# Performance work log

Measured on AMD Instinct MI355X. Metric: run time of the kernel, lower is better.

The kernel has to match this reference:

```python
import jax, jax.numpy as jnp
import numpy as np

HEAD_DIM = 64
N_HEADS = 32
N_KV_HEADS = 8
ROPE_THETA = 10000.0
NEG_INF = -1e9


def _rope_cos_sin(position_ids, head_dim, dtype):
    # position_ids: [b, s] int -> cos/sin [b, s, head_dim]
    inv_freq = 1.0 / (ROPE_THETA ** (jnp.arange(0, head_dim, 2, dtype=jnp.float32) / head_dim))
    freqs = position_ids.astype(jnp.float32)[..., None] * inv_freq  # [b, s, d/2]
    emb = jnp.concatenate([freqs, freqs], axis=-1)                  # [b, s, d]
    return jnp.cos(emb).astype(dtype), jnp.sin(emb).astype(dtype)


def _rotate_half(x):
    half = x.shape[-1] // 2
    return jnp.concatenate([-x[..., half:], x[..., :half]], axis=-1)


def setup_inputs() -> dict:
    key = jax.random.key(0)
    ks = jax.random.split(key, 6)
    b, s, din = 2, 2048, 4096  # din = 2 * hidden_size
    hidden_states = jax.random.normal(ks[0], (b, s, din), dtype=jnp.float32)
    # additive causal mask [b, 1, q, kv]
    causal = jnp.tril(jnp.ones((s, s), dtype=bool))
    attention_mask = jnp.where(causal, 0.0, NEG_INF).astype(jnp.float32)
    attention_mask = jnp.broadcast_to(attention_mask[None, None], (b, 1, s, s))
    position_ids = jnp.broadcast_to(jnp.arange(s, dtype=jnp.int32)[None], (b, s))
    scale = 0.02
    Wq = jax.random.normal(ks[1], (din, N_HEADS * HEAD_DIM), dtype=jnp.float32) * scale
    Wk = jax.random.normal(ks[2], (din, N_KV_HEADS * HEAD_DIM), dtype=jnp.float32) * scale
    Wv = jax.random.normal(ks[3], (din, N_KV_HEADS * HEAD_DIM), dtype=jnp.float32) * scale
    Wo = jax.random.normal(ks[4], (N_HEADS * HEAD_DIM, din // 2), dtype=jnp.float32) * scale
    return {"hidden_states": hidden_states, "attention_mask": attention_mask,
            "position_ids": position_ids, "Wq": Wq, "Wk": Wk, "Wv": Wv, "Wo": Wo}


def reference(hidden_states, attention_mask, position_ids, Wq, Wk, Wv, Wo):
    b, s, _ = hidden_states.shape
    g = N_HEADS // N_KV_HEADS  # GQA group size
    q = (hidden_states @ Wq).reshape(b, s, N_HEADS, HEAD_DIM).transpose(0, 2, 1, 3)      # [b,h,s,d]
    k = (hidden_states @ Wk).reshape(b, s, N_KV_HEADS, HEAD_DIM).transpose(0, 2, 1, 3)   # [b,kh,s,d]
    v = (hidden_states @ Wv).reshape(b, s, N_KV_HEADS, HEAD_DIM).transpose(0, 2, 1, 3)
    cos, sin = _rope_cos_sin(position_ids, HEAD_DIM, q.dtype)  # [b,s,d]
    cos, sin = cos[:, None], sin[:, None]                      # [b,1,s,d]
    q = q * cos + _rotate_half(q) * sin
    k = k * cos + _rotate_half(k) * sin
    # GQA: group query heads instead of materializing repeated K/V
    qg = q.reshape(b, N_KV_HEADS, g, s, HEAD_DIM)
    scores = jnp.einsum('bhgqd,bhkd->bhgqk', qg, k) / jnp.sqrt(jnp.float32(HEAD_DIM))
    scores = scores + attention_mask[:, :, None]               # broadcast over kv-head, group
    probs = jax.nn.softmax(scores.astype(jnp.float32), axis=-1).astype(q.dtype)
    out = jnp.einsum('bhgqk,bhkd->bhgqd', probs, v)            # [b,kh,g,s,d]
    out = out.reshape(b, N_HEADS, s, HEAD_DIM).transpose(0, 2, 1, 3).reshape(b, s, N_HEADS * HEAD_DIM)
    return out @ Wo
```

## Files before the change

### kernel.cpp

```cpp
#include <hip/hip_runtime.h>
#include <hip/hip_bf16.h>
#include <cstdint>
#include <cstddef>

typedef __attribute__((ext_vector_type(4))) float floatx4;
typedef __attribute__((ext_vector_type(8))) short shortx8;

typedef __attribute__((address_space(1))) void gvoid;
typedef __attribute__((address_space(3))) void lvoid;

__device__ inline __hip_bfloat16 f2b(float x) { return __float2bfloat16(x); }
__device__ inline float b2f(__hip_bfloat16 x) { return __bfloat162float(x); }
__device__ inline unsigned short f2bu(float x) {
  __hip_bfloat16 h = __float2bfloat16(x);
  return *reinterpret_cast<unsigned short*>(&h);
}
__device__ inline unsigned cvt_pk_bf16(float lo, float hi) {
  unsigned r;
  asm("v_cvt_pk_bf16_f32 %0, %1, %2" : "=v"(r) : "v"(lo), "v"(hi));
  return r;
}

template <typename T> __device__ inline T cvt_out(float x);
template <> __device__ inline float cvt_out<float>(float x) { return x; }
template <> __device__ inline __hip_bfloat16 cvt_out<__hip_bfloat16>(float x) { return __float2bfloat16(x); }

__global__ void cvt_f32_bf16(const float* __restrict__ in, __hip_bfloat16* __restrict__ out, int n) {
  int i = (blockIdx.x * blockDim.x + threadIdx.x) * 4;
  if (i >= n) return;
  float4 v = *(const float4*)(in + i);
  __hip_bfloat16 o[4] = { f2b(v.x), f2b(v.y), f2b(v.z), f2b(v.w) };
  *(ushort4*)(out + i) = *(const ushort4*)o;
}

__global__ void transpose_cvt(const float* __restrict__ in, __hip_bfloat16* __restrict__ out, int K, int N) {
  __shared__ float tile[32][33];
  int n0 = blockIdx.x * 32, k0 = blockIdx.y * 32;
  int tx = threadIdx.x, ty = threadIdx.y;
#pragma unroll
  for (int i = 0; i < 4; i++)
    tile[ty + i * 8][tx] = in[(size_t)(k0 + ty + i * 8) * N + n0 + tx];
  __syncthreads();
#pragma unroll
  for (int i = 0; i < 4; i++)
    out[(size_t)(n0 + ty + i * 8) * K + k0 + tx] = f2b(tile[tx][ty + i * 8]);
}

template <typename OutT>
__global__ __launch_bounds__(256) void gemm_bt(
    const __hip_bfloat16* __restrict__ A,
    const __hip_bfloat16* __restrict__ Bt,
    OutT* __restrict__ C, int M, int N, int K) {
  __shared__ short lA[128 * 32];
  __shared__ short lB[128 * 32];
  const int m0 = blockIdx.x * 128, n0 = blockIdx.y * 128;
  const int t = threadIdx.x;
  const int l = t & 63;
  const int w = t >> 6;
  const int wm = (w & 1) * 64, wn = (w >> 1) * 64;
  const int lr = l & 15, lq = l >> 4;
  floatx4 acc[4][4] = {};

  for (int kt = 0; kt < K; kt += 32) {
    __syncthreads();
#pragma unroll
    for (int j = 0; j < 2; j++) {
      int flat = j * 2048 + t * 8;
      const __hip_bfloat16* srcA = A + (size_t)(m0 + (flat >> 5)) * K + kt + (flat & 31);
      __builtin_amdgcn_global_load_lds((gvoid*)srcA, (lvoid*)&lA[flat], 16, 0, 0);
      const __hip_bfloat16* srcB = Bt + (size_t)(n0 + (flat >> 5)) * K + kt + (flat & 31);
      __builtin_amdgcn_global_load_lds((gvoid*)srcB, (lvoid*)&lB[flat], 16, 0, 0);
    }
    __syncthreads();
    shortx8 af[4], bfr[4];
#pragma unroll
    for (int mi = 0; mi < 4; mi++)
      af[mi] = *(const shortx8*)&lA[(wm + mi * 16 + lr) * 32 + lq * 8];
#pragma unroll
    for (int ni = 0; ni < 4; ni++)
      bfr[ni] = *(const shortx8*)&lB[(wn + ni * 16 + lr) * 32 + lq * 8];
#pragma unroll
    for (int mi = 0; mi < 4; mi++)
#pragma unroll
      for (int ni = 0; ni < 4; ni++)
        acc[mi][ni] = __builtin_amdgcn_mfma_f32_16x16x32_bf16(af[mi], bfr[ni], acc[mi][ni], 0, 0, 0);
  }
#pragma unroll
  for (int mi = 0; mi < 4; mi++)
#pragma unroll
    for (int ni = 0; ni < 4; ni++) {
      int row = m0 + wm + mi * 16 + lq * 4;
      int col = n0 + wn + ni * 16 + lr;
#pragma unroll
      for (int r = 0; r < 4; r++)
        C[(size_t)(row + r) * N + col] = cvt_out<OutT>(acc[mi][ni][r]);
    }
}

__global__ void rope_kernel(__hip_bfloat16* __restrict__ q, int stride, float scale) {
  int i = threadIdx.x;
  int row = blockIdx.x * 8 + threadIdx.y;
  int head = blockIdx.y;
  int pos = row & 2047;
  float freq = (float)pos * exp2f(-(float)i * (13.287712379549449f / 32.0f));
  float s = sinf(freq), c = cosf(freq);
  __hip_bfloat16* p = q + (size_t)row * stride + head * 64 + i;
  float x1 = b2f(p[0]), x2 = b2f(p[32]);
  p[0]  = f2b((x1 * c - x2 * s) * scale);
  p[32] = f2b((x2 * c + x1 * s) * scale);
}

__global__ void v_transpose(const __hip_bfloat16* __restrict__ QKV, __hip_bfloat16* __restrict__ Vt) {
  __shared__ __hip_bfloat16 tile[32][33];
  int bkvh = blockIdx.z;
  int s0 = blockIdx.x * 32, d0 = blockIdx.y * 32;
  int b = bkvh >> 3, kvh = bkvh & 7;
  int tx = threadIdx.x, ty = threadIdx.y;
#pragma unroll
  for (int i = 0; i < 4; i++)
    tile[ty + i * 8][tx] = QKV[(size_t)(b * 2048 + s0 + ty + i * 8) * 3072 + 2560 + kvh * 64 + d0 + tx];
  __syncthreads();
#pragma unroll
  for (int i = 0; i < 4; i++)
    Vt[((size_t)(bkvh * 64 + d0 + ty + i * 8) << 11) + s0 + tx] = tile[tx][ty + i * 8];
}

__global__ __launch_bounds__(256, 3) void attn_kernel(
    const __hip_bfloat16* __restrict__ Qp,
    const __hip_bfloat16* __restrict__ Kp,
    const __hip_bfloat16* __restrict__ Vt,
    __hip_bfloat16* __restrict__ O) {
  __shared__ __align__(16) short lK[2][64 * 64];
  __shared__ __align__(16) short lV[2][64 * 64];
  __shared__ __align__(16) short lP[4][16 * 64];
  const int h = blockIdx.y, b = blockIdx.z;
  const int ia = ((int)blockIdx.x + (h & 15) + ((h >> 4) << 3) + (b << 2)) & 15;
  const int ib = 31 - ia;
  const int kvh = h >> 2;
  const int t = threadIdx.x, w = t >> 6, l = t & 63;
  const int lr = l & 15, lq = l >> 4;
  const int swz = lr & 7;

  const int q0A = ia * 64 + w * 16;
  const int q0B = ib * 64 + w * 16;
  const __hip_bfloat16* qpA = Qp + (size_t)(b * 2048 + q0A + lr) * 3072 + h * 64 + lq * 8;
  const __hip_bfloat16* qpB = Qp + (size_t)(b * 2048 + q0B + lr) * 3072 + h * 64 + lq * 8;
  shortx8 qfA0 = *(const shortx8*)(qpA);
  shortx8 qfA1 = *(const shortx8*)(qpA + 32);
  shortx8 qfB0 = *(const shortx8*)(qpB);
  shortx8 qfB1 = *(const shortx8*)(qpB + 32);

  const int srow = t >> 3, schunk = t & 7;
  const int swzch = schunk ^ (srow & 7);
  const __hip_bfloat16* ksrc = Kp + (size_t)(b * 2048 + srow) * 3072 + kvh * 64 + swzch * 8;
  const __hip_bfloat16* vsrc = Vt + ((size_t)((b * 8 + kvh) * 64 + srow) << 11) + swzch * 8;
  short* const myP = &lP[w][0];

  floatx4 oA[4] = {}, oB[4] = {};
  float mA = -1e30f, sumA = 0.f, mB = -1e30f, sumB = 0.f;

  const int KT = 32 - ia;

  auto stage = [&](int sbuf, int kt2) {
#pragma unroll
    for (int j = 0; j < 2; j++) {
      __builtin_amdgcn_global_load_lds((gvoid*)(ksrc + (size_t)(kt2 * 64 + j * 32) * 3072),
                                       (lvoid*)&lK[sbuf][w * 512 + j * 2048], 16, 0, 0);
      __builtin_amdgcn_global_load_lds((gvoid*)(vsrc + (size_t)(j * 32) * 2048 + kt2 * 64),
                                       (lvoid*)&lV[sbuf][w * 512 + j * 2048], 16, 0, 0);
    }
  };

  stage(0, 0);

  for (int kt = 0; kt < KT; kt++) {
    const int buf = kt & 1;
    __syncthreads();
    if (kt + 1 < KT) stage(buf ^ 1, kt + 1);
    const bool doA = (kt <= ia);

    floatx4 sA[4] = {}, sB[4] = {};
    __builtin_amdgcn_s_setprio(1);
#pragma unroll
    for (int mi = 0; mi < 4; mi++) {
      const short* kr = &lK[buf][(mi * 16 + lr) * 64];
      shortx8 kf0 = *(const shortx8*)(kr + ((lq ^ swz) << 3));
      shortx8 kf1 = *(const shortx8*)(kr + (((4 + lq) ^ swz) << 3));
      if (doA) {
        sA[mi] = __builtin_amdgcn_mfma_f32_16x16x32_bf16(kf0, qfA0, sA[mi], 0, 0, 0);
        sA[mi] = __builtin_amdgcn_mfma_f32_16x16x32_bf16(kf1, qfA1, sA[mi], 0, 0, 0);
      }
      sB[mi] = __builtin_amdgcn_mfma_f32_16x16x32_bf16(kf0, qfB0, sB[mi], 0, 0, 0);
      sB[mi] = __builtin_amdgcn_mfma_f32_16x16x32_bf16(kf1, qfB1, sB[mi], 0, 0, 0);
    }
    __builtin_amdgcn_s_setprio(0);

    shortx8 pA0, pA1, pB0, pB1;
    float alphaA = 1.f, alphaB = 1.f;
    bool rescA = false, rescB = false;

    if (doA) {
      if (kt == ia) {
#pragma unroll
        for (int mi = 0; mi < 4; mi++)
#pragma unroll
          for (int r = 0; r < 4; r++)
            if (mi * 16 + lq * 4 + r > w * 16 + lr) sA[mi][r] = -3e8f;
      }
      float pm[4];
#pragma unroll
      for (int mi = 0; mi < 4; mi++)
        pm[mi] = fmaxf(fmaxf(sA[mi][0], sA[mi][1]), fmaxf(sA[mi][2], sA[mi][3]));
      float mx = fmaxf(fmaxf(pm[0], pm[1]), fmaxf(pm[2], pm[3]));
      mx = fmaxf(mx, __shfl_xor(mx, 16, 64));
      mx = fmaxf(mx, __shfl_xor(mx, 32, 64));
      rescA = !__all(mx <= mA + 8.f);
      if (rescA) {
        float mnew = fmaxf(mA, mx);
        alphaA = exp2f(mA - mnew);
        mA = mnew;
      }
      float rsm[4];
#pragma unroll
      for (int mi = 0; mi < 4; mi++) {
        float p0 = exp2f(sA[mi][0] - mA), p1 = exp2f(sA[mi][1] - mA);
        float p2 = exp2f(sA[mi][2] - mA), p3 = exp2f(sA[mi][3] - mA);
        sA[mi][0] = p0; sA[mi][1] = p1; sA[mi][2] = p2; sA[mi][3] = p3;
        rsm[mi] = (p0 + p1) + (p2 + p3);
      }
      float rs = (rsm[0] + rsm[1]) + (rsm[2] + rsm[3]);
      rs += __shfl_xor(rs, 16, 64);
      rs += __shfl_xor(rs, 32, 64);
      sumA = rescA ? sumA * alphaA + rs : sumA + rs;
#pragma unroll
      for (int mi = 0; mi < 4; mi++) {
        uint2 val;
        val.x = cvt_pk_bf16(sA[mi][0], sA[mi][1]);
        val.y = cvt_pk_bf16(sA[mi][2], sA[mi][3]);
        *(uint2*)(myP + lr * 64 + (((mi * 2 + (lq >> 1)) ^ swz) << 3) + ((lq & 1) << 2)) = val;
      }
      pA0 = *(const shortx8*)(myP + lr * 64 + ((lq ^ swz) << 3));
      pA1 = *(const shortx8*)(myP + lr * 64 + (((4 + lq) ^ swz) << 3));
    }

    {
      if (kt == KT - 1) {
#pragma unroll
        for (int mi = 0; mi < 4; mi++)
#pragma unroll
          for (int r = 0; r < 4; r++)
            if (mi * 16 + lq * 4 + r > w * 16 + lr) sB[mi][r] = -3e8f;
      }
      float pm[4];
#pragma unroll
      for (int mi = 0; mi < 4; mi++)
        pm[mi] = fmaxf(fmaxf(sB[mi][0], sB[mi][1]), fmaxf(sB[mi][2], sB[mi][3]));
      float mx = fmaxf(fmaxf(pm[0], pm[1]), fmaxf(pm[2], pm[3]));
      mx = fmaxf(mx, __shfl_xor(mx, 16, 64));
      mx = fmaxf(mx, __shfl_xor(mx, 32, 64));
      rescB = !__all(mx <= mB + 8.f);
      if (rescB) {
        float mnew = fmaxf(mB, mx);
        alphaB = exp2f(mB - mnew);
        mB = mnew;
      }
      float rsm[4];
#pragma unroll
      for (int mi = 0; mi < 4; mi++) {
        float p0 = exp2f(sB[mi][0] - mB), p1 = exp2f(sB[mi][1] - mB);
        float p2 = exp2f(sB[mi][2] - mB), p3 = exp2f(sB[mi][3] - mB);
        sB[mi][0] = p0; sB[mi][1] = p1; sB[mi][2] = p2; sB[mi][3] = p3;
        rsm[mi] = (p0 + p1) + (p2 + p3);
      }
      float rs = (rsm[0] + rsm[1]) + (rsm[2] + rsm[3]);
      rs += __shfl_xor(rs, 16, 64);
      rs += __shfl_xor(rs, 32, 64);
      sumB = rescB ? sumB * alphaB + rs : sumB + rs;
#pragma unroll
      for (int mi = 0; mi < 4; mi++) {
        uint2 val;
        val.x = cvt_pk_bf16(sB[mi][0], sB[mi][1]);
        val.y = cvt_pk_bf16(sB[mi][2], sB[mi][3]);
        *(uint2*)(myP + lr * 64 + (((mi * 2 + (lq >> 1)) ^ swz) << 3) + ((lq & 1) << 2)) = val;
      }
      pB0 = *(const shortx8*)(myP + lr * 64 + ((lq ^ swz) << 3));
      pB1 = *(const shortx8*)(myP + lr * 64 + (((4 + lq) ^ swz) << 3));
    }

    __builtin_amdgcn_s_setprio(1);
#pragma unroll
    for (int mi = 0; mi < 4; mi++) {
      const short* vr = &lV[buf][(mi * 16 + lr) * 64];
      shortx8 vf0 = *(const shortx8*)(vr + ((lq ^ swz) << 3));
      shortx8 vf1 = *(const shortx8*)(vr + (((4 + lq) ^ swz) << 3));
      if (doA) {
        floatx4 o = oA[mi];
        if (rescA) {
#pragma unroll
          for (int r = 0; r < 4; r++) o[r] *= alphaA;
        }
        o = __builtin_amdgcn_mfma_f32_16x16x32_bf16(vf0, pA0, o, 0, 0, 0);
        o = __builtin_amdgcn_mfma_f32_16x16x32_bf16(vf1, pA1, o, 0, 0, 0);
        oA[mi] = o;
      }
      floatx4 o2 = oB[mi];
      if (rescB) {
#pragma unroll
        for (int r = 0; r < 4; r++) o2[r] *= alphaB;
      }
      o2 = __builtin_amdgcn_mfma_f32_16x16x32_bf16(vf0, pB0, o2, 0, 0, 0);
      o2 = __builtin_amdgcn_mfma_f32_16x16x32_bf16(vf1, pB1, o2, 0, 0, 0);
      oB[mi] = o2;
    }
    __builtin_amdgcn_s_setprio(0);
  }

  const float livA = 1.f / sumA, livB = 1.f / sumB;
  __hip_bfloat16* obase = O + (size_t)(b * 2048 + q0A + lr) * 2048 + h * 64 + lq * 4;
#pragma unroll
  for (int mi = 0; mi < 4; mi++) {
    uint2 pk;
    pk.x = cvt_pk_bf16(oA[mi][0] * livA, oA[mi][1] * livA);
    pk.y = cvt_pk_bf16(oA[mi][2] * livA, oA[mi][3] * livA);
    *(uint2*)(obase + mi * 16) = pk;
  }
  __hip_bfloat16* obase2 = O + (size_t)(b * 2048 + q0B + lr) * 2048 + h * 64 + lq * 4;
#pragma unroll
  for (int mi = 0; mi < 4; mi++) {
    uint2 pk;
    pk.x = cvt_pk_bf16(oB[mi][0] * livB, oB[mi][1] * livB);
    pk.y = cvt_pk_bf16(oB[mi][2] * livB, oB[mi][3] * livB);
    *(uint2*)(obase2 + mi * 16) = pk;
  }
}

extern "C" void kernel_launch(void* const* d_in, const int* in_sizes, int n_in,
                              void* d_out, int out_size, void* d_ws, size_t ws_size,
                              hipStream_t stream) {
  (void)in_sizes; (void)n_in; (void)out_size; (void)ws_size;
  const float* hs = (const float*)d_in[0];
  const float* Wq = (const float*)d_in[3];
  const float* Wk = (const float*)d_in[4];
  const float* Wv = (const float*)d_in[5];
  const float* Wo = (const float*)d_in[6];
  float* out = (float*)d_out;

  char* p = (char*)d_ws;
  auto alloc = [&](size_t elts) { __hip_bfloat16* r = (__hip_bfloat16*)p; p += elts * 2; return r; };
  __hip_bfloat16* Xb   = alloc(4096ull * 4096);
  __hip_bfloat16* Wt   = alloc(3072ull * 4096);
  __hip_bfloat16* Wot  = alloc(2048ull * 2048);
  __hip_bfloat16* QKVb = alloc(4096ull * 3072);
  __hip_bfloat16* Vtb  = alloc(2ull * 8 * 64 * 2048);
  __hip_bfloat16* Ab   = alloc(4096ull * 2048);

  cvt_f32_bf16<<<16384, 256, 0, stream>>>(hs, Xb, 4096 * 4096);
  transpose_cvt<<<dim3(64, 128), dim3(32, 8), 0, stream>>>(Wq, Wt, 4096, 2048);
  transpose_cvt<<<dim3(16, 128), dim3(32, 8), 0, stream>>>(Wk, Wt + 2048ull * 4096, 4096, 512);
  transpose_cvt<<<dim3(16, 128), dim3(32, 8), 0, stream>>>(Wv, Wt + 2560ull * 4096, 4096, 512);
  transpose_cvt<<<dim3(64, 64), dim3(32, 8), 0, stream>>>(Wo, Wot, 2048, 2048);

  gemm_bt<__hip_bfloat16><<<dim3(32, 24), 256, 0, stream>>>(Xb, Wt, QKVb, 4096, 3072, 4096);

  rope_kernel<<<dim3(512, 32), dim3(32, 8), 0, stream>>>(QKVb, 3072, 0.18033688011112042f);
  rope_kernel<<<dim3(512, 8), dim3(32, 8), 0, stream>>>(QKVb + 2048, 3072, 1.0f);
  v_transpose<<<dim3(64, 2, 16), dim3(32, 8), 0, stream>>>(QKVb, Vtb);

  attn_kernel<<<dim3(16, 32, 2), 256, 0, stream>>>(QKVb, QKVb + 2048, Vtb, Ab);

  gemm_bt<float><<<dim3(32, 16), 256, 0, stream>>>(Ab, Wot, out, 4096, 2048, 2048);
}
```

Measured before the change: 557.9 us.

## Replace LDS P round-trip and shuffles with permlane swaps in attention softmax

Removes the per-wave LDS scratch buffer used to re-layout softmax probabilities into MFMA operand order. Instead, packed bf16 probabilities are rearranged in registers with v_permlane32_swap/v_permlane16_swap. Row-max reduction also switches from __shfl_xor (ds_bpermute) to permlane swaps. The row-sum cross-lane reduction is deferred from every tile to once at the end, which cuts LDS traffic and latency in the inner loop. The risk is that the register permutation must exactly reproduce the previous LDS layout, and it is gfx950-specific.

```diff
diff --git a/kernel.cpp b/kernel.cpp
--- a/kernel.cpp
+++ b/kernel.cpp
@@ -11,14 +11,35 @@
 
 __device__ inline __hip_bfloat16 f2b(float x) { return __float2bfloat16(x); }
 __device__ inline float b2f(__hip_bfloat16 x) { return __bfloat162float(x); }
-__device__ inline unsigned short f2bu(float x) {
-  __hip_bfloat16 h = __float2bfloat16(x);
-  return *reinterpret_cast<unsigned short*>(&h);
-}
 __device__ inline unsigned cvt_pk_bf16(float lo, float hi) {
   unsigned r;
   asm("v_cvt_pk_bf16_f32 %0, %1, %2" : "=v"(r) : "v"(lo), "v"(hi));
   return r;
+}
+__device__ inline unsigned vmov(unsigned a) {
+  unsigned r; asm("v_mov_b32 %0, %1" : "=v"(r) : "v"(a)); return r;
+}
+__device__ inline void plswap16(unsigned &a, unsigned &b) {
+  asm("v_permlane16_swap_b32 %0, %1" : "+v"(a), "+v"(b));
+}
+__device__ inline void plswap32(unsigned &a, unsigned &b) {
+  asm("v_permlane32_swap_b32 %0, %1" : "+v"(a), "+v"(b));
+}
+__device__ inline float red4_max(float v) {
+  unsigned a = __float_as_uint(v), b = vmov(a);
+  plswap16(a, b);
+  float m = fmaxf(__uint_as_float(a), __uint_as_float(b));
+  a = __float_as_uint(m); b = vmov(a);
+  plswap32(a, b);
+  return fmaxf(__uint_as_float(a), __uint_as_float(b));
+}
+__device__ inline float red4_sum(float v) {
+  unsigned a = __float_as_uint(v), b = vmov(a);
+  plswap16(a, b);
+  float s = __uint_as_float(a) + __uint_as_float(b);
+  a = __float_as_uint(s); b = vmov(a);
+  plswap32(a, b);
+  return __uint_as_float(a) + __uint_as_float(b);
 }
 
 template <typename T> __device__ inline T cvt_out(float x);
@@ -132,7 +153,6 @@
     __hip_bfloat16* __restrict__ O) {
   __shared__ __align__(16) short lK[2][64 * 64];
   __shared__ __align__(16) short lV[2][64 * 64];
-  __shared__ __align__(16) short lP[4][16 * 64];
   const int h = blockIdx.y, b = blockIdx.z;
   const int ia = ((int)blockIdx.x + (h & 15) + ((h >> 4) << 3) + (b << 2)) & 15;
   const int ib = 31 - ia;
@@ -154,7 +174,6 @@
   const int swzch = schunk ^ (srow & 7);
   const __hip_bfloat16* ksrc = Kp + (size_t)(b * 2048 + srow) * 3072 + kvh * 64 + swzch * 8;
   const __hip_bfloat16* vsrc = Vt + ((size_t)((b * 8 + kvh) * 64 + srow) << 11) + swzch * 8;
-  short* const myP = &lP[w][0];
 
   floatx4 oA[4] = {}, oB[4] = {};
   float mA = -1e30f, sumA = 0.f, mB = -1e30f, sumB = 0.f;
@@ -211,36 +230,34 @@
 #pragma unroll
       for (int mi = 0; mi < 4; mi++)
         pm[mi] = fmaxf(fmaxf(sA[mi][0], sA[mi][1]), fmaxf(sA[mi][2], sA[mi][3]));
-      float mx = fmaxf(fmaxf(pm[0], pm[1]), fmaxf(pm[2], pm[3]));
-      mx = fmaxf(mx, __shfl_xor(mx, 16, 64));
-      mx = fmaxf(mx, __shfl_xor(mx, 32, 64));
+      float mx = red4_max(fmaxf(fmaxf(pm[0], pm[1]), fmaxf(pm[2], pm[3])));
       rescA = !__all(mx <= mA + 8.f);
       if (rescA) {
         float mnew = fmaxf(mA, mx);
         alphaA = exp2f(mA - mnew);
         mA = mnew;
       }
-      float rsm[4];
+      float rs = 0.f;
 #pragma unroll
       for (int mi = 0; mi < 4; mi++) {
         float p0 = exp2f(sA[mi][0] - mA), p1 = exp2f(sA[mi][1] - mA);
         float p2 = exp2f(sA[mi][2] - mA), p3 = exp2f(sA[mi][3] - mA);
         sA[mi][0] = p0; sA[mi][1] = p1; sA[mi][2] = p2; sA[mi][3] = p3;
-        rsm[mi] = (p0 + p1) + (p2 + p3);
-      }
-      float rs = (rsm[0] + rsm[1]) + (rsm[2] + rsm[3]);
-      rs += __shfl_xor(rs, 16, 64);
-      rs += __shfl_xor(rs, 32, 64);
+        rs += (p0 + p1) + (p2 + p3);
+      }
       sumA = rescA ? sumA * alphaA + rs : sumA + rs;
+      unsigned Wm[4][2];
 #pragma unroll
       for (int mi = 0; mi < 4; mi++) {
-        uint2 val;
-        val.x = cvt_pk_bf16(sA[mi][0], sA[mi][1]);
-        val.y = cvt_pk_bf16(sA[mi][2], sA[mi][3]);
-        *(uint2*)(myP + lr * 64 + (((mi * 2 + (lq >> 1)) ^ swz) << 3) + ((lq & 1) << 2)) = val;
-      }
-      pA0 = *(const shortx8*)(myP + lr * 64 + ((lq ^ swz) << 3));
-      pA1 = *(const shortx8*)(myP + lr * 64 + (((4 + lq) ^ swz) << 3));
+        Wm[mi][0] = cvt_pk_bf16(sA[mi][0], sA[mi][1]);
+        Wm[mi][1] = cvt_pk_bf16(sA[mi][2], sA[mi][3]);
+      }
+      unsigned x0 = Wm[0][0], y0 = Wm[1][0]; plswap32(x0, y0); plswap16(x0, y0);
+      unsigned x1 = Wm[0][1], y1 = Wm[1][1]; plswap32(x1, y1); plswap16(x1, y1);
+      uint4 t0{x0, x1, y0, y1}; pA0 = *(const shortx8*)&t0;
+      unsigned x2 = Wm[2][0], y2 = Wm[3][0]; plswap32(x2, y2); plswap16(x2, y2);
+      unsigned x3 = Wm[2][1], y3 = Wm[3][1]; plswap32(x3, y3); plswap16(x3, y3);
+      uint4 t1{x2, x3, y2, y3}; pA1 = *(const shortx8*)&t1;
     }
 
     {
@@ -255,36 +272,34 @@
 #pragma unroll
       for (int mi = 0; mi < 4; mi++)
         pm[mi] = fmaxf(fmaxf(sB[mi][0], sB[mi][1]), fmaxf(sB[mi][2], sB[mi][3]));
-      float mx = fmaxf(fmaxf(pm[0], pm[1]), fmaxf(pm[2], pm[3]));
-      mx = fmaxf(mx, __shfl_xor(mx, 16, 64));
-      mx = fmaxf(mx, __shfl_xor(mx, 32, 64));
+      float mx = red4_max(fmaxf(fmaxf(pm[0], pm[1]), fmaxf(pm[2], pm[3])));
       rescB = !__all(mx <= mB + 8.f);
       if (rescB) {
         float mnew = fmaxf(mB, mx);
         alphaB = exp2f(mB - mnew);
         mB = mnew;
       }
-      float rsm[4];
+      float rs = 0.f;
 #pragma unroll
       for (int mi = 0; mi < 4; mi++) {
         float p0 = exp2f(sB[mi][0] - mB), p1 = exp2f(sB[mi][1] - mB);
         float p2 = exp2f(sB[mi][2] - mB), p3 = exp2f(sB[mi][3] - mB);
         sB[mi][0] = p0; sB[mi][1] = p1; sB[mi][2] = p2; sB[mi][3] = p3;
-        rsm[mi] = (p0 + p1) + (p2 + p3);
-      }
-      float rs = (rsm[0] + rsm[1]) + (rsm[2] + rsm[3]);
-      rs += __shfl_xor(rs, 16, 64);
-      rs += __shfl_xor(rs, 32, 64);
+        rs += (p0 + p1) + (p2 + p3);
+      }
       sumB = rescB ? sumB * alphaB + rs : sumB + rs;
+      unsigned Wm[4][2];
 #pragma unroll
       for (int mi = 0; mi < 4; mi++) {
-        uint2 val;
-        val.x = cvt_pk_bf16(sB[mi][0], sB[mi][1]);
-        val.y = cvt_pk_bf16(sB[mi][2], sB[mi][3]);
-        *(uint2*)(myP + lr * 64 + (((mi * 2 + (lq >> 1)) ^ swz) << 3) + ((lq & 1) << 2)) = val;
-      }
-      pB0 = *(const shortx8*)(myP + lr * 64 + ((lq ^ swz) << 3));
-      pB1 = *(const shortx8*)(myP + lr * 64 + (((4 + lq) ^ swz) << 3));
+        Wm[mi][0] = cvt_pk_bf16(sB[mi][0], sB[mi][1]);
+        Wm[mi][1] = cvt_pk_bf16(sB[mi][2], sB[mi][3]);
+      }
+      unsigned x0 = Wm[0][0], y0 = Wm[1][0]; plswap32(x0, y0); plswap16(x0, y0);
+      unsigned x1 = Wm[0][1], y1 = Wm[1][1]; plswap32(x1, y1); plswap16(x1, y1);
+      uint4 t0{x0, x1, y0, y1}; pB0 = *(const shortx8*)&t0;
+      unsigned x2 = Wm[2][0], y2 = Wm[3][0]; plswap32(x2, y2); plswap16(x2, y2);
+      unsigned x3 = Wm[2][1], y3 = Wm[3][1]; plswap32(x3, y3); plswap16(x3, y3);
+      uint4 t1{x2, x3, y2, y3}; pB1 = *(const shortx8*)&t1;
     }
 
     __builtin_amdgcn_s_setprio(1);
@@ -315,7 +330,7 @@
     __builtin_amdgcn_s_setprio(0);
   }
 
-  const float livA = 1.f / sumA, livB = 1.f / sumB;
+  const float livA = 1.f / red4_sum(sumA), livB = 1.f / red4_sum(sumB);
   __hip_bfloat16* obase = O + (size_t)(b * 2048 + q0A + lr) * 2048 + h * 64 + lq * 4;
 #pragma unroll
   for (int mi = 0; mi < 4; mi++) {
```

After: 524.7 us. 1.06x faster.
